# Optimization experiments

Measured on AMD Instinct MI355X. Metric: run time of the kernel, lower is better.

The kernel has to match this reference:

```python
import jax, jax.numpy as jnp
import numpy as np

BIG = 1e10  # stand-in for excluding masked rows from the min (safe for vjp)


def setup_inputs() -> dict:
    key = jax.random.key(0)
    k1, k2 = jax.random.split(key)
    # projected points: mostly inside the 640x480 image, some outside so the mask matters
    proj = jax.random.uniform(k1, (16384, 2), dtype=jnp.float32)
    proj = proj * jnp.array([700.0, 520.0], jnp.float32) - jnp.array([30.0, 20.0], jnp.float32)
    # reference centerline points, inside the image
    ref = jax.random.uniform(k2, (8192, 2), dtype=jnp.float32)
    ref = ref * jnp.array([640.0, 480.0], jnp.float32)
    return {"bezier_proj_centerline_img": proj, "ref_catheter_centerline": ref}


def reference(bezier_proj_centerline_img, ref_catheter_centerline):
    # torch .flip(1) on [M,2] swaps (x,y); .flip(0) on [N,2] reverses point order
    ref = ref_catheter_centerline[:, ::-1]            # [M, 2]
    proj = bezier_proj_centerline_img[::-1, :]        # [N, 2]

    # in-image mask (torch version drops rows; we keep static shapes and mask)
    mask = (
        (proj[:, 0] >= 0.0) & (proj[:, 0] <= 640.0)
        & (proj[:, 1] >= 0.0) & (proj[:, 1] <= 480.0)
    )  # [N]

    # pairwise L2 distances [N, M]
    diff = proj[:, None, :] - ref[None, :, :]         # [N, M, 2]
    dist = jnp.sqrt(jnp.sum(diff * diff, axis=-1))    # [N, M]

    # exclude invalid projected points from both reductions
    dist_masked = jnp.where(mask[:, None], dist, BIG)

    min1 = jnp.min(dist_masked, axis=1)               # [N] nearest ref per proj point
    n_valid = jnp.sum(mask.astype(dist.dtype))
    mean1 = jnp.sum(jnp.where(mask, min1, 0.0)) / n_valid

    min2 = jnp.min(dist_masked, axis=0)               # [M] nearest valid proj per ref point
    mean2 = jnp.mean(min2)

    return (mean1 + mean2) * 0.5
```

## Files before the change

kernel.cpp:

```cpp
#include <hip/hip_runtime.h>


constexpr int NP = 16384;
constexpr int NR = 8192;
constexpr int S1 = 16;
constexpr int S2 = 32;
constexpr int CHUNK = 512;
constexpr float FMAX = 3.4e38f;

__global__ __launch_bounds__(256) void k_prep(const float* __restrict__ proj,
                                              float* __restrict__ pm) {
    int i = blockIdx.x * 256 + threadIdx.x;
    float px = proj[2 * i], py = proj[2 * i + 1];
    bool valid = (px >= 0.f) && (px <= 640.f) && (py >= 0.f) && (py <= 480.f);
    pm[2 * i]     = valid ? px : 1e15f;
    pm[2 * i + 1] = valid ? py : 1e15f;
}

__global__ __launch_bounds__(256) void k_min1(const float* __restrict__ proj,
                                              const float* __restrict__ ref,
                                              float* __restrict__ min1p) {
    __shared__ float2 s[CHUNK];
    int tid = threadIdx.x;
    int i = blockIdx.x * 256 + tid;
    int c = blockIdx.y;
    float4 v = ((const float4*)(ref + 2 * c * CHUNK))[tid];
    s[2 * tid]     = make_float2(v.y, v.x);
    s[2 * tid + 1] = make_float2(v.w, v.z);
    __syncthreads();

    float2 p = ((const float2*)proj)[i];
    float m0 = FMAX, m1 = FMAX, m2 = FMAX, m3 = FMAX;
    for (int j = 0; j < CHUNK; j += 4) {
        float2 a = s[j], b = s[j + 1], cc = s[j + 2], d = s[j + 3];
        float dx0 = p.x - a.x,  dy0 = p.y - a.y;
        float dx1 = p.x - b.x,  dy1 = p.y - b.y;
        float dx2 = p.x - cc.x, dy2 = p.y - cc.y;
        float dx3 = p.x - d.x,  dy3 = p.y - d.y;
        m0 = fminf(m0, dx0 * dx0 + dy0 * dy0);
        m1 = fminf(m1, dx1 * dx1 + dy1 * dy1);
        m2 = fminf(m2, dx2 * dx2 + dy2 * dy2);
        m3 = fminf(m3, dx3 * dx3 + dy3 * dy3);
    }
    min1p[c * NP + i] = fminf(fminf(m0, m1), fminf(m2, m3));
}

__global__ __launch_bounds__(256) void k_min2(const float* __restrict__ ref,
                                              const float* __restrict__ pm,
                                              float* __restrict__ min2p) {
    __shared__ float2 s[CHUNK];
    int tid = threadIdx.x;
    int j = blockIdx.x * 256 + tid;
    int c = blockIdx.y;
    float4 v = ((const float4*)(pm + 2 * c * CHUNK))[tid];
    s[2 * tid]     = make_float2(v.x, v.y);
    s[2 * tid + 1] = make_float2(v.z, v.w);
    __syncthreads();

    float2 r = ((const float2*)ref)[j];
    float q0 = r.y, q1 = r.x;
    float m0 = FMAX, m1 = FMAX, m2 = FMAX, m3 = FMAX;
    for (int i = 0; i < CHUNK; i += 4) {
        float2 a = s[i], b = s[i + 1], cc = s[i + 2], d = s[i + 3];
        float dx0 = a.x - q0,  dy0 = a.y - q1;
        float dx1 = b.x - q0,  dy1 = b.y - q1;
        float dx2 = cc.x - q0, dy2 = cc.y - q1;
        float dx3 = d.x - q0,  dy3 = d.y - q1;
        m0 = fminf(m0, dx0 * dx0 + dy0 * dy0);
        m1 = fminf(m1, dx1 * dx1 + dy1 * dy1);
        m2 = fminf(m2, dx2 * dx2 + dy2 * dy2);
        m3 = fminf(m3, dx3 * dx3 + dy3 * dy3);
    }
    min2p[c * NR + j] = fminf(fminf(m0, m1), fminf(m2, m3));
}

__global__ __launch_bounds__(256) void k_combine(const float* __restrict__ proj,
                                                 const float* __restrict__ min1p,
                                                 const float* __restrict__ min2p,
                                                 float* __restrict__ bsum1,
                                                 float* __restrict__ bcnt1,
                                                 float* __restrict__ bsum2) {
    __shared__ float red[256];
    __shared__ float redc[256];
    int tid = threadIdx.x;
    int b = blockIdx.x;
    if (b < 64) {
        int i = b * 256 + tid;
        float m = FMAX;
        for (int ss = 0; ss < S1; ++ss) m = fminf(m, min1p[ss * NP + i]);
        float px = proj[2 * i], py = proj[2 * i + 1];
        bool valid = (px >= 0.f) && (px <= 640.f) && (py >= 0.f) && (py <= 480.f);
        red[tid]  = valid ? sqrtf(m) : 0.f;
        redc[tid] = valid ? 1.f : 0.f;
        __syncthreads();
        for (int w = 128; w > 0; w >>= 1) {
            if (tid < w) { red[tid] += red[tid + w]; redc[tid] += redc[tid + w]; }
            __syncthreads();
        }
        if (tid == 0) { bsum1[b] = red[0]; bcnt1[b] = redc[0]; }
    } else {
        int j = (b - 64) * 256 + tid;
        float m = FMAX;
        for (int ss = 0; ss < S2; ++ss) m = fminf(m, min2p[ss * NR + j]);
        red[tid] = sqrtf(m);
        __syncthreads();
        for (int w = 128; w > 0; w >>= 1) {
            if (tid < w) red[tid] += red[tid + w];
            __syncthreads();
        }
        if (tid == 0) bsum2[b - 64] = red[0];
    }
}

__global__ void k_final(const float* __restrict__ bsum1,
                        const float* __restrict__ bcnt1,
                        const float* __restrict__ bsum2,
                        float* __restrict__ out) {
    float s1 = 0.f, c1 = 0.f, s2 = 0.f;
    for (int b = 0; b < 64; ++b) { s1 += bsum1[b]; c1 += bcnt1[b]; }
    for (int b = 0; b < 32; ++b) s2 += bsum2[b];
    out[0] = 0.5f * (s1 / c1 + s2 / (float)NR);
}

extern "C" void kernel_launch(void* const* d_in, const int* in_sizes, int n_in,
                              void* d_out, int out_size, void* d_ws, size_t ws_size,
                              hipStream_t stream) {
    const float* proj = (const float*)d_in[0];
    const float* ref  = (const float*)d_in[1];
    float* out = (float*)d_out;

    float* ws    = (float*)d_ws;
    float* pm    = ws;
    float* min1p = pm + 2 * NP;
    float* min2p = min1p + S1 * NP;
    float* bsum1 = min2p + S2 * NR;
    float* bcnt1 = bsum1 + 64;
    float* bsum2 = bcnt1 + 64;

    k_prep<<<NP / 256, 256, 0, stream>>>(proj, pm);
    k_min1<<<dim3(NP / 256, S1), 256, 0, stream>>>(proj, ref, min1p);
    k_min2<<<dim3(NR / 256, S2), 256, 0, stream>>>(ref, pm, min2p);
    k_combine<<<96, 256, 0, stream>>>(proj, min1p, min2p, bsum1, bcnt1, bsum2);
    k_final<<<1, 1, 0, stream>>>(bsum1, bcnt1, bsum2, out);
}
```

Baseline: 45.34 us.

## Expand squared distance into dot-product form and merge both min passes

Precomputes per-point keys (-2x, -2y, |p|^2) so each pair costs two FMAs plus a min, and adds the query norm back before the sqrt in the combine stage. The two pairwise kernels become one launch, and each thread handles four query points against a 256-key shared tile for more register reuse. This cuts per-pair ALU work and one kernel launch, but the expanded form can lose precision through cancellation, and the partial buffers grow because the chunks are smaller.

```diff
diff --git a/kernel.cpp b/kernel.cpp
--- a/kernel.cpp
+++ b/kernel.cpp
@@ -3,80 +3,107 @@
 
 constexpr int NP = 16384;
 constexpr int NR = 8192;
-constexpr int S1 = 16;
-constexpr int S2 = 32;
-constexpr int CHUNK = 512;
+constexpr int CH = 256;
+constexpr int S1 = NR / CH;
+constexpr int S2 = NP / CH;
+constexpr int BLK1 = NP / 1024;
+constexpr int BLK2 = NR / 1024;
+constexpr int G1 = BLK1 * S1;
+constexpr int G2 = BLK2 * S2;
 constexpr float FMAX = 3.4e38f;
 
 __global__ __launch_bounds__(256) void k_prep(const float* __restrict__ proj,
-                                              float* __restrict__ pm) {
+                                              const float* __restrict__ ref,
+                                              float4* __restrict__ kproj,
+                                              float4* __restrict__ kref) {
     int i = blockIdx.x * 256 + threadIdx.x;
-    float px = proj[2 * i], py = proj[2 * i + 1];
-    bool valid = (px >= 0.f) && (px <= 640.f) && (py >= 0.f) && (py <= 480.f);
-    pm[2 * i]     = valid ? px : 1e15f;
-    pm[2 * i + 1] = valid ? py : 1e15f;
+    float2 p = ((const float2*)proj)[i];
+    bool valid = (p.x >= 0.f) && (p.x <= 640.f) && (p.y >= 0.f) && (p.y <= 480.f);
+    float pc = fmaf(p.x, p.x, p.y * p.y);
+    kproj[i] = valid ? make_float4(-2.f * p.x, -2.f * p.y, pc, 0.f)
+                     : make_float4(0.f, 0.f, 1e30f, 0.f);
+    if (i < NR) {
+        float2 r = ((const float2*)ref)[i];
+        kref[i] = make_float4(-2.f * r.y, -2.f * r.x, fmaf(r.x, r.x, r.y * r.y), 0.f);
+    }
 }
 
-__global__ __launch_bounds__(256) void k_min1(const float* __restrict__ proj,
+__global__ __launch_bounds__(256) void k_pair(const float* __restrict__ proj,
                                               const float* __restrict__ ref,
-                                              float* __restrict__ min1p) {
-    __shared__ float2 s[CHUNK];
+                                              const float4* __restrict__ kproj,
+                                              const float4* __restrict__ kref,
+                                              float* __restrict__ part1,
+                                              float* __restrict__ part2) {
+    __shared__ float4 sh[CH];
     int tid = threadIdx.x;
-    int i = blockIdx.x * 256 + tid;
-    int c = blockIdx.y;
-    float4 v = ((const float4*)(ref + 2 * c * CHUNK))[tid];
-    s[2 * tid]     = make_float2(v.y, v.x);
-    s[2 * tid + 1] = make_float2(v.w, v.z);
+    int bx = blockIdx.x;
+    bool d1 = bx < G1;
+    int cb = d1 ? bx : bx - G1;
+    int nbm = (d1 ? BLK1 : BLK2) - 1;
+    int pb = cb & nbm;
+    int ck = cb >> (d1 ? 4 : 3);
+
+    const float4* keys = d1 ? kref : kproj;
+    sh[tid] = keys[ck * CH + tid];
     __syncthreads();
 
-    float2 p = ((const float2*)proj)[i];
-    float m0 = FMAX, m1 = FMAX, m2 = FMAX, m3 = FMAX;
-    for (int j = 0; j < CHUNK; j += 4) {
-        float2 a = s[j], b = s[j + 1], cc = s[j + 2], d = s[j + 3];
-        float dx0 = p.x - a.x,  dy0 = p.y - a.y;
-        float dx1 = p.x - b.x,  dy1 = p.y - b.y;
-        float dx2 = p.x - cc.x, dy2 = p.y - cc.y;
-        float dx3 = p.x - d.x,  dy3 = p.y - d.y;
-        m0 = fminf(m0, dx0 * dx0 + dy0 * dy0);
-        m1 = fminf(m1, dx1 * dx1 + dy1 * dy1);
-        m2 = fminf(m2, dx2 * dx2 + dy2 * dy2);
-        m3 = fminf(m3, dx3 * dx3 + dy3 * dy3);
+    int base = pb * 1024 + tid;
+    const float2* qsrc = (const float2*)(d1 ? proj : ref);
+    float2 q0 = qsrc[base];
+    float2 q1 = qsrc[base + 256];
+    float2 q2 = qsrc[base + 512];
+    float2 q3 = qsrc[base + 768];
+    if (!d1) {
+        float t;
+        t = q0.x; q0.x = q0.y; q0.y = t;
+        t = q1.x; q1.x = q1.y; q1.y = t;
+        t = q2.x; q2.x = q2.y; q2.y = t;
+        t = q3.x; q3.x = q3.y; q3.y = t;
     }
-    min1p[c * NP + i] = fminf(fminf(m0, m1), fminf(m2, m3));
-}
 
-__global__ __launch_bounds__(256) void k_min2(const float* __restrict__ ref,
-                                              const float* __restrict__ pm,
-                                              float* __restrict__ min2p) {
-    __shared__ float2 s[CHUNK];
-    int tid = threadIdx.x;
-    int j = blockIdx.x * 256 + tid;
-    int c = blockIdx.y;
-    float4 v = ((const float4*)(pm + 2 * c * CHUNK))[tid];
-    s[2 * tid]     = make_float2(v.x, v.y);
-    s[2 * tid + 1] = make_float2(v.z, v.w);
-    __syncthreads();
+    float ma0 = FMAX, mb0 = FMAX, ma1 = FMAX, mb1 = FMAX;
+    float ma2 = FMAX, mb2 = FMAX, ma3 = FMAX, mb3 = FMAX;
+#pragma unroll 4
+    for (int j = 0; j < CH; j += 4) {
+        float4 k0 = sh[j], k1 = sh[j + 1], k2 = sh[j + 2], k3 = sh[j + 3];
+        float t00 = fmaf(k0.y, q0.y, fmaf(k0.x, q0.x, k0.z));
+        float t01 = fmaf(k1.y, q0.y, fmaf(k1.x, q0.x, k1.z));
+        float t02 = fmaf(k2.y, q0.y, fmaf(k2.x, q0.x, k2.z));
+        float t03 = fmaf(k3.y, q0.y, fmaf(k3.x, q0.x, k3.z));
+        ma0 = fminf(fminf(ma0, t00), t01);
+        mb0 = fminf(fminf(mb0, t02), t03);
+        float t10 = fmaf(k0.y, q1.y, fmaf(k0.x, q1.x, k0.z));
+        float t11 = fmaf(k1.y, q1.y, fmaf(k1.x, q1.x, k1.z));
+        float t12 = fmaf(k2.y, q1.y, fmaf(k2.x, q1.x, k2.z));
+        float t13 = fmaf(k3.y, q1.y, fmaf(k3.x, q1.x, k3.z));
+        ma1 = fminf(fminf(ma1, t10), t11);
+        mb1 = fminf(fminf(mb1, t12), t13);
+        float t20 = fmaf(k0.y, q2.y, fmaf(k0.x, q2.x, k0.z));
+        float t21 = fmaf(k1.y, q2.y, fmaf(k1.x, q2.x, k1.z));
+        float t22 = fmaf(k2.y, q2.y, fmaf(k2.x, q2.x, k2.z));
+        float t23 = fmaf(k3.y, q2.y, fmaf(k3.x, q2.x, k3.z));
+        ma2 = fminf(fminf(ma2, t20), t21);
+        mb2 = fminf(fminf(mb2, t22), t23);
+        float t30 = fmaf(k0.y, q3.y, fmaf(k0.x, q3.x, k0.z));
+        float t31 = fmaf(k1.y, q3.y, fmaf(k1.x, q3.x, k1.z));
+        float t32 = fmaf(k2.y, q3.y, fmaf(k2.x, q3.x, k2.z));
+        float t33 = fmaf(k3.y, q3.y, fmaf(k3.x, q3.x, k3.z));
+        ma3 = fminf(fminf(ma3, t30), t31);
+        mb3 = fminf(fminf(mb3, t32), t33);
+    }
 
-    float2 r = ((const float2*)ref)[j];
-    float q0 = r.y, q1 = r.x;
-    float m0 = FMAX, m1 = FMAX, m2 = FMAX, m3 = FMAX;
-    for (int i = 0; i < CHUNK; i += 4) {
-        float2 a = s[i], b = s[i + 1], cc = s[i + 2], d = s[i + 3];
-        float dx0 = a.x - q0,  dy0 = a.y - q1;
-        float dx1 = b.x - q0,  dy1 = b.y - q1;
-        float dx2 = cc.x - q0, dy2 = cc.y - q1;
-        float dx3 = d.x - q0,  dy3 = d.y - q1;
-        m0 = fminf(m0, dx0 * dx0 + dy0 * dy0);
-        m1 = fminf(m1, dx1 * dx1 + dy1 * dy1);
-        m2 = fminf(m2, dx2 * dx2 + dy2 * dy2);
-        m3 = fminf(m3, dx3 * dx3 + dy3 * dy3);
-    }
-    min2p[c * NR + j] = fminf(fminf(m0, m1), fminf(m2, m3));
+    float* part = d1 ? part1 : part2;
+    int n = d1 ? NP : NR;
+    part[ck * n + base]       = fminf(ma0, mb0);
+    part[ck * n + base + 256] = fminf(ma1, mb1);
+    part[ck * n + base + 512] = fminf(ma2, mb2);
+    part[ck * n + base + 768] = fminf(ma3, mb3);
 }
 
 __global__ __launch_bounds__(256) void k_combine(const float* __restrict__ proj,
-                                                 const float* __restrict__ min1p,
-                                                 const float* __restrict__ min2p,
+                                                 const float* __restrict__ ref,
+                                                 const float* __restrict__ part1,
+                                                 const float* __restrict__ part2,
                                                  float* __restrict__ bsum1,
                                                  float* __restrict__ bcnt1,
                                                  float* __restrict__ bsum2) {
@@ -87,10 +114,11 @@
     if (b < 64) {
         int i = b * 256 + tid;
         float m = FMAX;
-        for (int ss = 0; ss < S1; ++ss) m = fminf(m, min1p[ss * NP + i]);
-        float px = proj[2 * i], py = proj[2 * i + 1];
-        bool valid = (px >= 0.f) && (px <= 640.f) && (py >= 0.f) && (py <= 480.f);
-        red[tid]  = valid ? sqrtf(m) : 0.f;
+        for (int c = 0; c < S1; ++c) m = fminf(m, part1[c * NP + i]);
+        float2 p = ((const float2*)proj)[i];
+        bool valid = (p.x >= 0.f) && (p.x <= 640.f) && (p.y >= 0.f) && (p.y <= 480.f);
+        float d = sqrtf(fmaxf(m + fmaf(p.x, p.x, p.y * p.y), 0.f));
+        red[tid]  = valid ? d : 0.f;
         redc[tid] = valid ? 1.f : 0.f;
         __syncthreads();
         for (int w = 128; w > 0; w >>= 1) {
@@ -101,8 +129,9 @@
     } else {
         int j = (b - 64) * 256 + tid;
         float m = FMAX;
-        for (int ss = 0; ss < S2; ++ss) m = fminf(m, min2p[ss * NR + j]);
-        red[tid] = sqrtf(m);
+        for (int c = 0; c < S2; ++c) m = fminf(m, part2[c * NR + j]);
+        float2 r = ((const float2*)ref)[j];
+        red[tid] = sqrtf(fmaxf(m + fmaf(r.x, r.x, r.y * r.y), 0.f));
         __syncthreads();
         for (int w = 128; w > 0; w >>= 1) {
             if (tid < w) red[tid] += red[tid + w];
@@ -129,17 +158,17 @@
     const float* ref  = (const float*)d_in[1];
     float* out = (float*)d_out;
 
-    float* ws    = (float*)d_ws;
-    float* pm    = ws;
-    float* min1p = pm + 2 * NP;
-    float* min2p = min1p + S1 * NP;
-    float* bsum1 = min2p + S2 * NR;
-    float* bcnt1 = bsum1 + 64;
-    float* bsum2 = bcnt1 + 64;
+    float* ws = (float*)d_ws;
+    float4* kproj = (float4*)ws;
+    float4* kref  = kproj + NP;
+    float*  part1 = (float*)(kref + NR);
+    float*  part2 = part1 + S1 * NP;
+    float*  bsum1 = part2 + S2 * NR;
+    float*  bcnt1 = bsum1 + 64;
+    float*  bsum2 = bcnt1 + 64;
 
-    k_prep<<<NP / 256, 256, 0, stream>>>(proj, pm);
-    k_min1<<<dim3(NP / 256, S1), 256, 0, stream>>>(proj, ref, min1p);
-    k_min2<<<dim3(NR / 256, S2), 256, 0, stream>>>(ref, pm, min2p);
-    k_combine<<<96, 256, 0, stream>>>(proj, min1p, min2p, bsum1, bcnt1, bsum2);
+    k_prep<<<NP / 256, 256, 0, stream>>>(proj, ref, kproj, kref);
+    k_pair<<<G1 + G2, 256, 0, stream>>>(proj, ref, kproj, kref, part1, part2);
+    k_combine<<<96, 256, 0, stream>>>(proj, ref, part1, part2, bsum1, bcnt1, bsum2);
     k_final<<<1, 1, 0, stream>>>(bsum1, bcnt1, bsum2, out);
 }
```

Measured after the change: 45.54 us. Within noise of the previous version (+0.4%).
